# Optimization experiments

Measured on AMD Instinct MI355X. Metric: run time of the kernel, lower is better.

The kernel has to match this reference:

```python
import jax, jax.numpy as jnp
import numpy as np
import math

B, S, D, H, WIDTH, NHW = 8, 1024, 512, 8, 8, 2
DK = D // H
S2 = S + 2 * WIDTH


def setup_inputs() -> dict:
    key = jax.random.key(0)
    ks = jax.random.split(key, 12)
    sc = 1.0 / math.sqrt(D)
    return {
        "x": jax.random.normal(ks[0], (B, S, D), jnp.float32),
        "l_attn_W": jax.random.normal(ks[1], (4, D, D), jnp.float32) * sc,  # q,k,v,out
        "l_attn_b": jnp.zeros((4, D), jnp.float32),
        "r_attn_W": jax.random.normal(ks[2], (4, D, D), jnp.float32) * sc,
        "r_attn_b": jnp.zeros((4, D), jnp.float32),
        "left_pad": jax.random.normal(ks[3], (WIDTH, D), jnp.float32) * sc,
        "right_pad": jax.random.normal(ks[4], (WIDTH, D), jnp.float32) * sc,
        "left_w": jax.random.normal(ks[5], (WIDTH + 1,), jnp.float32),
        "right_w": jax.random.normal(ks[6], (WIDTH + 1,), jnp.float32),
        "l_hw_W": jax.random.normal(ks[7], (NHW, D, 2 * D), jnp.float32) * sc,
        "l_hw_b": jnp.zeros((NHW, 2 * D), jnp.float32),
        "r_hw_W": jax.random.normal(ks[8], (NHW, D, 2 * D), jnp.float32) * sc,
        "r_hw_b": jnp.zeros((NHW, 2 * D), jnp.float32),
    }


def _mha(x, W, b, mask):
    # x: [B, S2, D]; W: [4, D, D]; mask: [1, S2, S2] bool (True = keep)
    q = (x @ W[0] + b[0]).reshape(B, S2, H, DK)
    k = (x @ W[1] + b[1]).reshape(B, S2, H, DK)
    v = (x @ W[2] + b[2]).reshape(B, S2, H, DK)
    scores = jnp.einsum('bihd,bjhd->bhij', q, k) / math.sqrt(DK)
    scores = jnp.where(mask[:, None], scores, jnp.float32(-1e9))
    p = jax.nn.softmax(scores, axis=-1)
    o = jnp.einsum('bhij,bjhd->bihd', p, v).reshape(B, S2, D)
    return o @ W[3] + b[3]


def _highway(x, Ws, bs):
    # AllenNLP-style Highway: projected -> [nonlinear | gate]
    for i in range(NHW):
        proj = x @ Ws[i] + bs[i]
        nl = jax.nn.relu(proj[..., :D])
        g = jax.nn.sigmoid(proj[..., D:])
        x = g * x + (1.0 - g) * nl
    return x


def reference(x, l_attn_W, l_attn_b, r_attn_W, r_attn_b, left_pad, right_pad,
              left_w, right_w, l_hw_W, l_hw_b, r_hw_W, r_hw_b):
    new_in = jnp.concatenate([
        jnp.broadcast_to(left_pad, (B, WIDTH, D)), x,
        jnp.broadcast_to(right_pad, (B, WIDTH, D))], axis=1)  # [B, S2, D]
    idx = jnp.arange(S2)
    diff = idx[:, None] - idx[None, :]
    lmask = ((diff >= 0) & (diff <= WIDTH + 1))[None]          # attend to [i-width-1, i]
    rmask = ((diff <= 0) & (diff >= -(WIDTH + 1)))[None]       # attend to [i, i+width+1]
    nl_attn = _mha(new_in, l_attn_W, l_attn_b, lmask)
    nr_attn = _mha(new_in, r_attn_W, r_attn_b, rmask)
    left_out = nl_attn[:, WIDTH:WIDTH + S, :]   # position end = start + width
    right_out = nr_attn[:, WIDTH:WIDTH + S, :]
    # relative-position weighted sliding windows (vectorized over all steps)
    lrel = sum(left_w[j] * new_in[:, j:j + S, :] for j in range(WIDTH + 1))
    rrel = sum(right_w[j] * new_in[:, WIDTH + j:WIDTH + j + S, :] for j in range(WIDTH + 1))
    left_out = _highway(left_out + lrel, l_hw_W, l_hw_b)
    right_out = _highway(right_out + rrel, r_hw_W, r_hw_b)
    out = jnp.concatenate([left_out, right_out], axis=-1)  # [B, S, 2D]
    return out[None]  # [1, B, S, 2D] matching torch stack layout
```

## Files before the change

### kernel.cpp

```cpp
#include <hip/hip_runtime.h>


#define B_ 8
#define S_ 1024
#define D_ 512
#define H_ 8
#define DK_ 64
#define WIDTH_ 8
#define S2_ 1040
#define NHW_ 2

typedef short bf16x8 __attribute__((ext_vector_type(8)));
typedef float f32x4 __attribute__((ext_vector_type(4)));

__device__ __forceinline__ float us2f(unsigned short u) {
  union { unsigned int i; float f; } c; c.i = ((unsigned int)u) << 16; return c.f;
}
__device__ __forceinline__ unsigned short f2us(float f) {
  union { float f; unsigned int i; } c; c.f = f;
  unsigned int x = c.i;
  return (unsigned short)((x + 0x7fffu + ((x >> 16) & 1u)) >> 16);
}
__device__ __forceinline__ unsigned int pack2(float a, float b) {
  return (unsigned int)f2us(a) | ((unsigned int)f2us(b) << 16);
}
__device__ __forceinline__ void async16(const void* g, void* l) {
  __builtin_amdgcn_global_load_lds(
      (const __attribute__((address_space(1))) void*)g,
      (__attribute__((address_space(3))) void*)l, 16, 0, 0);
}
__device__ __forceinline__ void unpack8(uint4 u, float* f) {
  unsigned int w[4] = {u.x, u.y, u.z, u.w};
  #pragma unroll
  for (int c = 0; c < 4; ++c) {
    union { unsigned int i; float g; } lo, hi;
    lo.i = w[c] << 16;
    hi.i = w[c] & 0xffff0000u;
    f[2 * c] = lo.g;
    f[2 * c + 1] = hi.g;
  }
}

__global__ __launch_bounds__(256) void k_prep(
    const float* __restrict__ x,
    const float* __restrict__ lpad, const float* __restrict__ rpad,
    const float* __restrict__ lW, const float* __restrict__ rW,
    const float* __restrict__ lb, const float* __restrict__ rb,
    const float* __restrict__ lhwW, const float* __restrict__ rhwW,
    unsigned short* __restrict__ WTall, unsigned short* __restrict__ WTp,
    unsigned short* __restrict__ hWT,
    unsigned short* __restrict__ nin, float* __restrict__ qkvbias)
{
  __shared__ float tile[32][33];
  const size_t DD = (size_t)D_ * D_;
  int bx = blockIdx.x;
  int tx = threadIdx.x & 31, ty = threadIdx.x >> 5;

  if (bx < 2048) {
    int sl = bx >> 8, rem = bx & 255;
    int side = sl >> 2, slice = sl & 3;
    int c0 = (rem & 15) * 32, r0 = (rem >> 4) * 32;
    const float* src = (side ? rW : lW) + (size_t)slice * DD;
    unsigned short* dst = (slice < 3) ? WTall + (size_t)(side * 3 + slice) * DD
                                      : WTp + (size_t)side * DD;
    #pragma unroll
    for (int i = 0; i < 4; ++i)
      tile[ty + i * 8][tx] = src[(size_t)(r0 + ty + i * 8) * D_ + c0 + tx];
    __syncthreads();
    #pragma unroll
    for (int i = 0; i < 4; ++i)
      dst[(size_t)(c0 + ty + i * 8) * D_ + r0 + tx] = f2us(tile[tx][ty + i * 8]);
    return;
  }
  if (bx < 4096) {
    int idx = bx - 2048;
    int sl = idx >> 9, rem = idx & 511;
    int c0 = (rem & 31) * 32, r0 = (rem >> 5) * 32;
    const float* src = ((sl >> 1) ? rhwW : lhwW) + (size_t)(sl & 1) * 512 * 1024;
    unsigned short* dst = hWT + (size_t)sl * 1024 * 512;
    #pragma unroll
    for (int i = 0; i < 4; ++i)
      tile[ty + i * 8][tx] = src[(size_t)(r0 + ty + i * 8) * 1024 + c0 + tx];
    __syncthreads();
    #pragma unroll
    for (int i = 0; i < 4; ++i) {
      int c = c0 + ty + i * 8;
      int cm = c & 511;
      int j = cm >> 4;
      int jl = j & 7;
      int Bq = ((jl >> 2) << 3) + (jl & 3) + ((c >= 512) ? 4 : 0);
      int q = (j >> 3) * 256 + Bq * 16 + (cm & 15);
      dst[(size_t)q * 512 + r0 + tx] = f2us(tile[tx][ty + i * 8]);
    }
    return;
  }
  int gid = (bx - 4096) * 256 + threadIdx.x;
  const int NTH = B_ * S2_ * 64;
  if (gid >= NTH) {
    int t = gid - NTH;
    if (t < 1536) qkvbias[t] = lb[t];
    else if (t < 3072) qkvbias[t] = rb[t - 1536];
    return;
  }
  int c8 = (gid & 63) << 3;
  int row = gid >> 6;
  int b = row / S2_;
  int t = row - b * S2_;
  const float* src;
  if (t < WIDTH_)            src = lpad + (size_t)t * D_ + c8;
  else if (t >= S_ + WIDTH_) src = rpad + (size_t)(t - S_ - WIDTH_) * D_ + c8;
  else                       src = x + ((size_t)b * S_ + (t - WIDTH_)) * D_ + c8;
  float4 a = *reinterpret_cast<const float4*>(src);
  float4 c = *reinterpret_cast<const float4*>(src + 4);
  uint4 o;
  o.x = pack2(a.x, a.y); o.y = pack2(a.z, a.w);
  o.z = pack2(c.x, c.y); o.w = pack2(c.z, c.w);
  *reinterpret_cast<uint4*>(nin + (size_t)row * D_ + c8) = o;
}

__global__ __launch_bounds__(256) void k_gemm_mfma(
    const unsigned short* __restrict__ A,
    const unsigned short* __restrict__ BT,
    const float* __restrict__ bias,
    unsigned short* __restrict__ C,
    int M, int N, int K)
{
  __shared__ unsigned short As[128 * 64];
  __shared__ unsigned short Bs[128 * 64];

  const int tid = threadIdx.x;
  const int w = tid >> 6;
  const int l = tid & 63;
  const int bm = blockIdx.y * 128;
  const int bn = blockIdx.x * 128;
  const int wrow = (w >> 1) * 64;
  const int wcol = (w & 1) * 64;

  const int lr = l >> 3;
  const int sk = (((l & 7) ^ lr) & 7) * 8;
  const unsigned short* Ap = A + (size_t)(bm + w * 8 + lr) * K + sk;
  const unsigned short* Bp = BT + (size_t)(bn + w * 8 + lr) * K + sk;
  unsigned short* lA = &As[w * 512];
  unsigned short* lB = &Bs[w * 512];
  const size_t K32 = (size_t)32 * K;

  const int fl = l & 15;
  const int fq = l >> 4;
  const int fx = fl & 7;

  f32x4 acc[4][4];
  #pragma unroll
  for (int mi = 0; mi < 4; ++mi)
    #pragma unroll
    for (int ni = 0; ni < 4; ++ni) acc[mi][ni] = (f32x4){0.f, 0.f, 0.f, 0.f};

  for (int k0 = 0; k0 < K; k0 += 64) {
    #pragma unroll
    for (int r = 0; r < 4; ++r) {
      async16(Ap + k0 + r * K32, lA + r * 2048);
      async16(Bp + k0 + r * K32, lB + r * 2048);
    }
    __syncthreads();
    #pragma unroll
    for (int s = 0; s < 2; ++s) {
      bf16x8 af[4], bfr[4];
      #pragma unroll
      for (int mi = 0; mi < 4; ++mi)
        af[mi] = *reinterpret_cast<const bf16x8*>(
            &As[(wrow + mi * 16 + fl) * 64 + (((s * 4 + fq) ^ fx) * 8)]);
      #pragma unroll
      for (int ni = 0; ni < 4; ++ni)
        bfr[ni] = *reinterpret_cast<const bf16x8*>(
            &Bs[(wcol + ni * 16 + fl) * 64 + (((s * 4 + fq) ^ fx) * 8)]);
      #pragma unroll
      for (int mi = 0; mi < 4; ++mi)
        #pragma unroll
        for (int ni = 0; ni < 4; ++ni)
          acc[mi][ni] = __builtin_amdgcn_mfma_f32_16x16x32_bf16(
              af[mi], bfr[ni], acc[mi][ni], 0, 0, 0);
    }
    __syncthreads();
  }

  float bv[4];
  #pragma unroll
  for (int ni = 0; ni < 4; ++ni) bv[ni] = bias[bn + wcol + ni * 16 + fl];

  const int rbase = (l >> 4) * 4;
  #pragma unroll
  for (int mi = 0; mi < 4; ++mi) {
    #pragma unroll
    for (int r = 0; r < 4; ++r) {
      int row = bm + wrow + mi * 16 + rbase + r;
      unsigned short* Cp = C + (size_t)row * N + bn + wcol + fl;
      #pragma unroll
      for (int ni = 0; ni < 4; ++ni)
        Cp[ni * 16] = f2us(acc[mi][ni][r] + bv[ni]);
    }
  }
}

template <int EPI>
__global__ __launch_bounds__(512, 2) void k_gemm256(
    const unsigned short* __restrict__ Abase, size_t aStrZ,
    const unsigned short* __restrict__ BTbase, size_t bStrZ,
    const float* __restrict__ bias0, const float* __restrict__ bias1,
    unsigned short* __restrict__ Cbf, float* __restrict__ Cfp,
    int M, int N)
{
  __shared__ __align__(16) unsigned short smem[65536];
  const int tid = threadIdx.x;
  const int w = tid >> 6, l = tid & 63;
  const int wm = w >> 2, wn = w & 3;
  const int fl = l & 15, fq = l >> 4;
  const int z = blockIdx.z;
  const unsigned short* A = Abase + (size_t)z * aStrZ;
  const unsigned short* BT = BTbase + (size_t)z * bStrZ;
  const int bm = blockIdx.y * 256, bn = blockIdx.x * 256;

  const int xorb = (fl & 7) << 4;
  const int cs0 = ((fq * 16) ^ xorb) >> 1;
  const int cs1 = ((64 + fq * 16) ^ xorb) >> 1;

  const int rr = l >> 3;
  const int ce = (((l & 7) * 16) ^ (rr << 4)) >> 1;
  const unsigned short* gA[2][2];
  const unsigned short* gB[2][2];
  #pragma unroll
  for (int i = 0; i < 2; ++i)
    #pragma unroll
    for (int h = 0; h < 2; ++h) {
      int ra = bm + h * 128 + (2 * w + i) * 8 + rr;
      if (ra > M - 1) ra = M - 1;
      gA[i][h] = A + (size_t)ra * 512 + ce;
      int rb = bn + h * 128 + (2 * w + i) * 8 + rr;
      gB[i][h] = BT + (size_t)rb * 512 + ce;
    }

  f32x4 acc[8][4];
  #pragma unroll
  for (int mi = 0; mi < 8; ++mi)
    #pragma unroll
    for (int ni = 0; ni < 4; ++ni) acc[mi][ni] = (f32x4){0.f, 0.f, 0.f, 0.f};

  bf16x8 ar[4][2], br[2][2];

#define BAR() __builtin_amdgcn_s_barrier()
#define STGA(buf, h, kt) do { \
    async16(gA[0][h] + (kt) * 64, &smem[((buf) * 2 + (h)) * 8192 + (2 * w) * 512]); \
    async16(gA[1][h] + (kt) * 64, &smem[((buf) * 2 + (h)) * 8192 + (2 * w + 1) * 512]); } while (0)
#define STGB(buf, h, kt) do { \
    async16(gB[0][h] + (kt) * 64, &smem[32768 + ((buf) * 2 + (h)) * 8192 + (2 * w) * 512]); \
    async16(gB[1][h] + (kt) * 64, &smem[32768 + ((buf) * 2 + (h)) * 8192 + (2 * w + 1) * 512]); } while (0)
#define LDA(buf, h) do { const unsigned short* p_ = &smem[((buf) * 2 + (h)) * 8192]; \
    _Pragma("unroll") for (int m4 = 0; m4 < 4; ++m4) { \
      int ro_ = ((2 * m4 + wm) * 16 + fl) * 64; \
      ar[m4][0] = *reinterpret_cast<const bf16x8*>(p_ + ro_ + cs0); \
      ar[m4][1] = *reinterpret_cast<const bf16x8*>(p_ + ro_ + cs1); } } while (0)
#define LDB(buf, h) do { const unsigned short* p_ = &smem[32768 + ((buf) * 2 + (h)) * 8192]; \
    _Pragma("unroll") for (int n2 = 0; n2 < 2; ++n2) { \
      int ro_ = ((4 * n2 + wn) * 16 + fl) * 64; \
      br[n2][0] = *reinterpret_cast<const bf16x8*>(p_ + ro_ + cs0); \
      br[n2][1] = *reinterpret_cast<const bf16x8*>(p_ + ro_ + cs1); } } while (0)
#define QUAD(miH, niH) do { __builtin_amdgcn_s_setprio(1); \
    _Pragma("unroll") for (int m4 = 0; m4 < 4; ++m4) \
      _Pragma("unroll") for (int n2 = 0; n2 < 2; ++n2) \
        _Pragma("unroll") for (int s_ = 0; s_ < 2; ++s_) \
          acc[(miH) * 4 + m4][(niH) * 2 + n2] = __builtin_amdgcn_mfma_f32_16x16x32_bf16( \
              ar[m4][s_], br[n2][s_], acc[(miH) * 4 + m4][(niH) * 2 + n2], 0, 0, 0); \
    __builtin_amdgcn_s_setprio(0); } while (0)

  STGA(0, 0, 0); STGB(0, 0, 0); STGB(0, 1, 0); STGA(0, 1, 0);
  STGA(1, 0, 1); STGB(1, 1, 1); STGA(1, 1, 1);
  asm volatile("s_waitcnt vmcnt(6)" ::: "memory");
  BAR();

  #pragma unroll 1
  for (int it = 0; it < 4; ++it) {
    const int t1 = 2 * it + 1, t2 = 2 * it + 2, t3 = 2 * it + 3;
    LDA(0, 0); LDB(0, 0);
    STGB(1, 0, t1);
    BAR(); QUAD(0, 0); BAR();
    LDB(0, 1);
    if (t2 < 8) STGA(0, 0, t2);
    BAR(); QUAD(0, 1); BAR();
    LDA(0, 1);
    if (t2 < 8) STGB(0, 1, t2);
    BAR(); QUAD(1, 1); BAR();
    LDB(0, 0);
    if (t2 < 8) STGA(0, 1, t2);
    BAR(); QUAD(1, 0);
    if (it < 3) asm volatile("s_waitcnt vmcnt(6)" ::: "memory");
    else        asm volatile("s_waitcnt vmcnt(0)" ::: "memory");
    BAR();
    LDA(1, 0); LDB(1, 0);
    if (t2 < 8) STGB(0, 0, t2);
    BAR(); QUAD(0, 0); BAR();
    LDB(1, 1);
    if (t3 < 8) STGA(1, 0, t3);
    BAR(); QUAD(0, 1); BAR();
    LDA(1, 1);
    if (t3 < 8) STGB(1, 1, t3);
    BAR(); QUAD(1, 1); BAR();
    LDB(1, 0);
    if (t3 < 8) STGA(1, 1, t3);
    BAR(); QUAD(1, 0);
    asm volatile("s_waitcnt vmcnt(6)" ::: "memory");
    BAR();
  }
#undef BAR
#undef STGA
#undef STGB
#undef LDA
#undef LDB
#undef QUAD

  {
    const float* bias = z ? bias1 : bias0;
    const size_t MS = (size_t)B_ * S_ * D_;
    float bnl[2], bg[2]; int xs[2];
    #pragma unroll
    for (int np = 0; np < 2; ++np) {
      xs[np] = (blockIdx.x * 8 + np * 4 + wn) * 16 + fl;
      bnl[np] = bias[xs[np]];
      bg[np]  = bias[512 + xs[np]];
    }
    #pragma unroll
    for (int mi = 0; mi < 8; ++mi) {
      #pragma unroll
      for (int r = 0; r < 4; ++r) {
        int gr = bm + (2 * mi + wm) * 16 + fq * 4 + r;
        #pragma unroll
        for (int np = 0; np < 2; ++np) {
          float nl = fmaxf(acc[mi][2 * np][r] + bnl[np], 0.f);
          float g  = 1.f / (1.f + __expf(-(acc[mi][2 * np + 1][r] + bg[np])));
          float xv = us2f(A[(size_t)gr * 512 + xs[np]]);
          float res = g * xv + (1.f - g) * nl;
          if (EPI == 2) Cfp[(size_t)gr * 1024 + (size_t)z * 512 + xs[np]] = res;
          else Cbf[(size_t)z * MS + (size_t)gr * 512 + xs[np]] = f2us(res);
        }
      }
    }
  }
}

__global__ __launch_bounds__(256) void k_gemm_proj(
    const unsigned short* __restrict__ ctx,
    const unsigned short* __restrict__ WTp,
    const unsigned short* __restrict__ nin,
    const float* __restrict__ lb3, const float* __restrict__ rb3,
    const float* __restrict__ wrel0, const float* __restrict__ wrel1,
    unsigned short* __restrict__ hwx)
{
  __shared__ unsigned short smem[128 * 136];
  unsigned short* As = smem;
  unsigned short* Bs = smem + 8192;
  const int K = 512, N = 512;
  const size_t MS = (size_t)B_ * S_ * D_;

  const int z = blockIdx.z;
  const unsigned short* A = ctx + (size_t)z * MS;
  const unsigned short* BT = WTp + (size_t)z * 512 * 512;
  const float* bias = z ? rb3 : lb3;
  const float* wrel = z ? wrel1 : wrel0;
  const int off = z * WIDTH_;

  const int tid = threadIdx.x;
  const int w = tid >> 6;
  const int l = tid & 63;
  const int bm = blockIdx.y * 128;
  const int bn = blockIdx.x * 128;
  const int wrow = (w >> 1) * 64;
  const int wcol = (w & 1) * 64;

  const int lr = l >> 3;
  const int sk = (((l & 7) ^ lr) & 7) * 8;
  const unsigned short* Ap = A + (size_t)(bm + w * 8 + lr) * K + sk;
  const unsigned short* Bp = BT + (size_t)(bn + w * 8 + lr) * K + sk;
  unsigned short* lA = &As[w * 512];
  unsigned short* lB = &Bs[w * 512];
  const size_t K32 = (size_t)32 * K;

  const int fl = l & 15;
  const int fq = l >> 4;
  const int fx = fl & 7;

  f32x4 acc[4][4];
  #pragma unroll
  for (int mi = 0; mi < 4; ++mi)
    #pragma unroll
    for (int ni = 0; ni < 4; ++ni) acc[mi][ni] = (f32x4){0.f, 0.f, 0.f, 0.f};

  for (int k0 = 0; k0 < K; k0 += 64) {
    #pragma unroll
    for (int r = 0; r < 4; ++r) {
      async16(Ap + k0 + r * K32, lA + r * 2048);
      async16(Bp + k0 + r * K32, lB + r * 2048);
    }
    __syncthreads();
    #pragma unroll
    for (int s = 0; s < 2; ++s) {
      bf16x8 af[4], bfr[4];
      #pragma unroll
      for (int mi = 0; mi < 4; ++mi)
        af[mi] = *reinterpret_cast<const bf16x8*>(
            &As[(wrow + mi * 16 + fl) * 64 + (((s * 4 + fq) ^ fx) * 8)]);
      #pragma unroll
      for (int ni = 0; ni < 4; ++ni)
        bfr[ni] = *reinterpret_cast<const bf16x8*>(
            &Bs[(wcol + ni * 16 + fl) * 64 + (((s * 4 + fq) ^ fx) * 8)]);
      #pragma unroll
      for (int mi = 0; mi < 4; ++mi)
        #pragma unroll
        for (int ni = 0; ni < 4; ++ni)
          acc[mi][ni] = __builtin_amdgcn_mfma_f32_16x16x32_bf16(
              af[mi], bfr[ni], acc[mi][ni], 0, 0, 0);
    }
    __syncthreads();
  }

  float bv[4];
  #pragma unroll
  for (int ni = 0; ni < 4; ++ni) bv[ni] = bias[bn + wcol + ni * 16 + fl];
  const int rbase = (l >> 4) * 4;
  #pragma unroll
  for (int mi = 0; mi < 4; ++mi)
    #pragma unroll
    for (int r = 0; r < 4; ++r)
      #pragma unroll
      for (int ni = 0; ni < 4; ++ni)
        smem[(wrow + mi * 16 + rbase + r) * 136 + wcol + ni * 16 + fl] =
            f2us(acc[mi][ni][r] + bv[ni]);
  __syncthreads();

  const int trow = tid >> 4;
  const int tcol = (tid & 15) * 8;
  const float w0 = wrel[0], w1 = wrel[1], w2 = wrel[2], w3 = wrel[3],
              w4 = wrel[4], w5 = wrel[5], w6 = wrel[6], w7 = wrel[7],
              w8 = wrel[8];
  const float wj[9] = {w0, w1, w2, w3, w4, w5, w6, w7, w8};
  #pragma unroll
  for (int i = 0; i < 8; ++i) {
    int r = trow + i * 16;
    int gr = bm + r;
    int b = gr >> 10, s = gr & (S_ - 1);
    float a8[8];
    unpack8(*reinterpret_cast<const uint4*>(&smem[r * 136 + tcol]), a8);
    const unsigned short* np =
        nin + ((size_t)b * S2_ + off + s) * D_ + bn + tcol;
    #pragma unroll
    for (int j = 0; j < 9; ++j) {
      float nf[8];
      unpack8(*reinterpret_cast<const uint4*>(np + (size_t)j * D_), nf);
      #pragma unroll
      for (int e = 0; e < 8; ++e) a8[e] += wj[j] * nf[e];
    }
    uint4 o;
    o.x = pack2(a8[0], a8[1]); o.y = pack2(a8[2], a8[3]);
    o.z = pack2(a8[4], a8[5]); o.w = pack2(a8[6], a8[7]);
    *reinterpret_cast<uint4*>(
        hwx + (size_t)z * MS + (size_t)gr * D_ + bn + tcol) = o;
  }
}

__global__ __launch_bounds__(256) void k_attn_window(
    const unsigned short* __restrict__ qkv,
    unsigned short* __restrict__ ctx)
{
  int wid = (blockIdx.x * 256 + threadIdx.x) >> 6;
  int lane = threadIdx.x & 63;
  int s = wid & (S_ - 1);
  int b = (wid >> 10) & (B_ - 1);
  int dir = wid >> 13;
  int i = s + WIDTH_;

  const size_t base = (size_t)b * S2_ * 3072 + dir * 1536;
  const int c0 = lane * 8;

  float qf[8];
  unpack8(*reinterpret_cast<const uint4*>(qkv + base + (size_t)i * 3072 + c0), qf);

  float sc[10];
  float mx = -1e30f;
  #pragma unroll
  for (int t = 0; t < 10; ++t) {
    int j = (dir == 0) ? (i - 9 + t) : (i + t);
    float sv = -1e30f;
    if (j >= 0 && j < S2_) {
      float kf[8];
      unpack8(*reinterpret_cast<const uint4*>(
          qkv + base + (size_t)j * 3072 + 512 + c0), kf);
      float p = qf[0] * kf[0];
      #pragma unroll
      for (int e = 1; e < 8; ++e) p += qf[e] * kf[e];
      p += __shfl_xor(p, 1);
      p += __shfl_xor(p, 2);
      p += __shfl_xor(p, 4);
      sv = p * 0.125f;
    }
    sc[t] = sv;
    mx = fmaxf(mx, sv);
  }

  float denom = 0.f;
  #pragma unroll
  for (int t = 0; t < 10; ++t) {
    sc[t] = (sc[t] > -1e29f) ? __expf(sc[t] - mx) : 0.f;
    denom += sc[t];
  }
  float inv = 1.f / denom;

  float acc[8] = {0.f, 0.f, 0.f, 0.f, 0.f, 0.f, 0.f, 0.f};
  #pragma unroll
  for (int t = 0; t < 10; ++t) {
    int j = (dir == 0) ? (i - 9 + t) : (i + t);
    if (j >= 0 && j < S2_) {
      float vf[8];
      unpack8(*reinterpret_cast<const uint4*>(
          qkv + base + (size_t)j * 3072 + 1024 + c0), vf);
      float p = sc[t];
      #pragma unroll
      for (int e = 0; e < 8; ++e) acc[e] += p * vf[e];
    }
  }

  uint4 o;
  o.x = pack2(acc[0] * inv, acc[1] * inv);
  o.y = pack2(acc[2] * inv, acc[3] * inv);
  o.z = pack2(acc[4] * inv, acc[5] * inv);
  o.w = pack2(acc[6] * inv, acc[7] * inv);
  *reinterpret_cast<uint4*>(
      ctx + (((size_t)dir * B_ + b) * S_ + s) * D_ + c0) = o;
}

extern "C" void kernel_launch(void* const* d_in, const int* in_sizes, int n_in,
                              void* d_out, int out_size, void* d_ws, size_t ws_size,
                              hipStream_t stream) {
  const float* x    = (const float*)d_in[0];
  const float* lW   = (const float*)d_in[1];
  const float* lb   = (const float*)d_in[2];
  const float* rW   = (const float*)d_in[3];
  const float* rb   = (const float*)d_in[4];
  const float* lpad = (const float*)d_in[5];
  const float* rpad = (const float*)d_in[6];
  const float* lw   = (const float*)d_in[7];
  const float* rw   = (const float*)d_in[8];
  const float* lhwW = (const float*)d_in[9];
  const float* lhwb = (const float*)d_in[10];
  const float* rhwW = (const float*)d_in[11];
  const float* rhwb = (const float*)d_in[12];
  float* out = (float*)d_out;
  unsigned short* ws = (unsigned short*)d_ws;

  const size_t NIN  = (size_t)B_ * S2_ * D_;
  const size_t NQKV = (size_t)B_ * S2_ * 3072;
  const size_t MS   = (size_t)B_ * S_ * D_;
  const size_t DD   = (size_t)D_ * D_;
  const size_t LHW  = (size_t)1024 * 512;

  unsigned short* nin   = ws;
  unsigned short* qkv   = nin + NIN;
  unsigned short* ctx   = qkv + NQKV;
  unsigned short* hwx   = ctx + 2 * MS;
  unsigned short* hwy   = hwx + 2 * MS;
  unsigned short* WTall = hwy + 2 * MS;
  unsigned short* WTp   = WTall + 6 * DD;
  unsigned short* hWT   = WTp + 2 * DD;
  float* qkvbias        = (float*)(hWT + 4 * LHW);

  k_prep<<<6188, 256, 0, stream>>>(x, lpad, rpad, lW, rW, lb, rb, lhwW, rhwW,
                                   WTall, WTp, hWT, nin, qkvbias);

  const int MQ = B_ * S2_;

  {
    dim3 g(3072 / 128, MQ / 128, 1);
    k_gemm_mfma<<<g, 256, 0, stream>>>(nin, WTall, qkvbias, qkv, MQ, 3072, D_);
  }

  k_attn_window<<<(2 * B_ * S_) / 4, 256, 0, stream>>>(qkv, ctx);

  {
    dim3 g(D_ / 128, (B_ * S_) / 128, 2);
    k_gemm_proj<<<g, 256, 0, stream>>>(ctx, WTp, nin, lb + 3 * D_, rb + 3 * D_,
                                       lw, rw, hwx);
  }

  {
    dim3 g(1024 / 256, (B_ * S_) / 256, 2);
    k_gemm256<1><<<g, 512, 0, stream>>>(hwx, MS, hWT, 2 * LHW,
                                        lhwb, rhwb, hwy, nullptr,
                                        B_ * S_, 1024);
    k_gemm256<2><<<g, 512, 0, stream>>>(hwy, MS, hWT + LHW, 2 * LHW,
                                        lhwb + 1024, rhwb + 1024,
                                        nullptr, out, B_ * S_, 1024);
  }
}
```

Baseline: 235.4 us.

## Process four query rows per wave in window attention and remap GEMM blocks per XCD

Each wavefront in the sliding-window attention kernel now handles four consecutive query positions. The overlapping K and V rows are loaded once and reused across those queries, which reduces global loads per output row. The QKV GEMM remaps its flat block index so consecutive tiles land on the same XCD for better L2 locality. The cost is higher register pressure in the attention kernel and fewer blocks launched.

```diff
diff --git a/kernel.cpp b/kernel.cpp
--- a/kernel.cpp
+++ b/kernel.cpp
@@ -131,8 +131,15 @@
   const int tid = threadIdx.x;
   const int w = tid >> 6;
   const int l = tid & 63;
-  const int bm = blockIdx.y * 128;
-  const int bn = blockIdx.x * 128;
+
+  const int gx = gridDim.x;
+  const int nwg = gx * gridDim.y;
+  const int flat = blockIdx.y * gx + blockIdx.x;
+  const int cpx = nwg >> 3;
+  const int nf = (flat & 7) * cpx + (flat >> 3);
+  const int bm = (nf / gx) * 128;
+  const int bn = (nf % gx) * 128;
+
   const int wrow = (w >> 1) * 64;
   const int wcol = (w & 1) * 64;
 
@@ -469,68 +476,96 @@
 {
   int wid = (blockIdx.x * 256 + threadIdx.x) >> 6;
   int lane = threadIdx.x & 63;
-  int s = wid & (S_ - 1);
-  int b = (wid >> 10) & (B_ - 1);
-  int dir = wid >> 13;
-  int i = s + WIDTH_;
+  int sg = wid & 255;
+  int b = (wid >> 8) & 7;
+  int dir = wid >> 11;
+  int s0 = sg << 2;
+  int i0 = s0 + WIDTH_;
 
   const size_t base = (size_t)b * S2_ * 3072 + dir * 1536;
   const int c0 = lane * 8;
 
-  float qf[8];
-  unpack8(*reinterpret_cast<const uint4*>(qkv + base + (size_t)i * 3072 + c0), qf);
-
-  float sc[10];
-  float mx = -1e30f;
-  #pragma unroll
-  for (int t = 0; t < 10; ++t) {
-    int j = (dir == 0) ? (i - 9 + t) : (i + t);
-    float sv = -1e30f;
-    if (j >= 0 && j < S2_) {
-      float kf[8];
+  float qf[4][8];
+  #pragma unroll
+  for (int r = 0; r < 4; ++r)
+    unpack8(*reinterpret_cast<const uint4*>(
+        qkv + base + (size_t)(i0 + r) * 3072 + c0), qf[r]);
+
+  float sc[4][10];
+  float mx[4] = {-1e30f, -1e30f, -1e30f, -1e30f};
+  #pragma unroll
+  for (int t = 0; t < 13; ++t) {
+    int j = (dir == 0) ? (i0 - 9 + t) : (i0 + t);
+    bool ok = (j >= 0 && j < S2_);
+    float kf[8];
+    if (ok)
       unpack8(*reinterpret_cast<const uint4*>(
           qkv + base + (size_t)j * 3072 + 512 + c0), kf);
-      float p = qf[0] * kf[0];
-      #pragma unroll
-      for (int e = 1; e < 8; ++e) p += qf[e] * kf[e];
-      p += __shfl_xor(p, 1);
-      p += __shfl_xor(p, 2);
-      p += __shfl_xor(p, 4);
-      sv = p * 0.125f;
-    }
-    sc[t] = sv;
-    mx = fmaxf(mx, sv);
-  }
-
-  float denom = 0.f;
-  #pragma unroll
-  for (int t = 0; t < 10; ++t) {
-    sc[t] = (sc[t] > -1e29f) ? __expf(sc[t] - mx) : 0.f;
-    denom += sc[t];
-  }
-  float inv = 1.f / denom;
-
-  float acc[8] = {0.f, 0.f, 0.f, 0.f, 0.f, 0.f, 0.f, 0.f};
-  #pragma unroll
-  for (int t = 0; t < 10; ++t) {
-    int j = (dir == 0) ? (i - 9 + t) : (i + t);
-    if (j >= 0 && j < S2_) {
-      float vf[8];
+    #pragma unroll
+    for (int r = 0; r < 4; ++r) {
+      if (t < r || t > r + 9) continue;
+      float sv = -1e30f;
+      if (ok) {
+        float p = qf[r][0] * kf[0];
+        #pragma unroll
+        for (int e = 1; e < 8; ++e) p += qf[r][e] * kf[e];
+        p += __shfl_xor(p, 1);
+        p += __shfl_xor(p, 2);
+        p += __shfl_xor(p, 4);
+        sv = p * 0.125f;
+      }
+      sc[r][t - r] = sv;
+      mx[r] = fmaxf(mx[r], sv);
+    }
+  }
+
+  float inv[4];
+  #pragma unroll
+  for (int r = 0; r < 4; ++r) {
+    float den = 0.f;
+    #pragma unroll
+    for (int u = 0; u < 10; ++u) {
+      sc[r][u] = (sc[r][u] > -1e29f) ? __expf(sc[r][u] - mx[r]) : 0.f;
+      den += sc[r][u];
+    }
+    inv[r] = 1.f / den;
+  }
+
+  float acc[4][8];
+  #pragma unroll
+  for (int r = 0; r < 4; ++r)
+    #pragma unroll
+    for (int e = 0; e < 8; ++e) acc[r][e] = 0.f;
+
+  #pragma unroll
+  for (int t = 0; t < 13; ++t) {
+    int j = (dir == 0) ? (i0 - 9 + t) : (i0 + t);
+    bool ok = (j >= 0 && j < S2_);
+    float vf[8];
+    if (ok)
       unpack8(*reinterpret_cast<const uint4*>(
           qkv + base + (size_t)j * 3072 + 1024 + c0), vf);
-      float p = sc[t];
-      #pragma unroll
-      for (int e = 0; e < 8; ++e) acc[e] += p * vf[e];
-    }
-  }
-
-  uint4 o;
-  o.x = pack2(acc[0] * inv, acc[1] * inv);
-  o.y = pack2(acc[2] * inv, acc[3] * inv);
-  o.z = pack2(acc[4] * inv, acc[5] * inv);
-  o.w = pack2(acc[6] * inv, acc[7] * inv);
-  *reinterpret_cast<uint4*>(
-      ctx + (((size_t)dir * B_ + b) * S_ + s) * D_ + c0) = o;
+    #pragma unroll
+    for (int r = 0; r < 4; ++r) {
+      if (t < r || t > r + 9) continue;
+      if (ok) {
+        float p = sc[r][t - r];
+        #pragma unroll
+        for (int e = 0; e < 8; ++e) acc[r][e] += p * vf[e];
+      }
+    }
+  }
+
+  #pragma unroll
+  for (int r = 0; r < 4; ++r) {
+    uint4 o;
+    o.x = pack2(acc[r][0] * inv[r], acc[r][1] * inv[r]);
+    o.y = pack2(acc[r][2] * inv[r], acc[r][3] * inv[r]);
+    o.z = pack2(acc[r][4] * inv[r], acc[r][5] * inv[r]);
+    o.w = pack2(acc[r][6] * inv[r], acc[r][7] * inv[r]);
+    *reinterpret_cast<uint4*>(
+        ctx + (((size_t)dir * B_ + b) * S_ + s0 + r) * D_ + c0) = o;
+  }
 }
 
 extern "C" void kernel_launch(void* const* d_in, const int* in_sizes, int n_in,
@@ -578,7 +613,7 @@
     k_gemm_mfma<<<g, 256, 0, stream>>>(nin, WTall, qkvbias, qkv, MQ, 3072, D_);
   }
 
-  k_attn_window<<<(2 * B_ * S_) / 4, 256, 0, stream>>>(qkv, ctx);
+  k_attn_window<<<(2 * B_ * S_) / 16, 256, 0, stream>>>(qkv, ctx);
 
   {
     dim3 g(D_ / 128, (B_ * S_) / 128, 2);
```

Result: no change. 236.4 us (+0.4%).
